# Optimization experiments

Hardware: AMD Instinct MI355X
Metric: run time of the kernel (lower is better)

The kernel has to match this reference:

```python
import math
import jax, jax.numpy as jnp
import numpy as np

# ---------- static Cl(3,0,0) algebra tables ----------
_BLADES = [(), (1,), (2,), (3,), (1, 2), (1, 3), (2, 3), (1, 2, 3)]
N_BLADES = 8
SUBSPACES = np.array([1, 3, 3, 1])
GRADE = np.array([len(b) for b in _BLADES])  # blade index -> grade

def _blade_mul(a, b):
    idx = list(a) + list(b)
    sign = 1
    changed = True
    while changed:
        changed = False
        for t in range(len(idx) - 1):
            if idx[t] > idx[t + 1]:
                idx[t], idx[t + 1] = idx[t + 1], idx[t]
                sign = -sign
                changed = True
    out = []
    t = 0
    while t < len(idx):
        if t + 1 < len(idx) and idx[t] == idx[t + 1]:
            t += 2  # e_i e_i = +1 (Euclidean metric)
        else:
            out.append(idx[t]); t += 1
    return sign, tuple(out)

# cayley[i, j, k]: e_i * e_k contributes sign to blade j (matches einsum 'bni,nijk,bnk->bnj')
CAYLEY = np.zeros((N_BLADES, N_BLADES, N_BLADES), dtype=np.float32)
for i, ba in enumerate(_BLADES):
    for k, bb in enumerate(_BLADES):
        s, res = _blade_mul(ba, bb)
        CAYLEY[i, _BLADES.index(res), k] = s

_starts = np.concatenate([[0], np.cumsum(SUBSPACES)[:-1]])
_paths = np.zeros((4, 4, 4), dtype=bool)
for gi in range(4):
    for gj in range(4):
        for gk in range(4):
            si, sj, sk = _starts[gi], _starts[gj], _starts[gk]
            blk = CAYLEY[si:si + SUBSPACES[gi], sj:sj + SUBSPACES[gj], sk:sk + SUBSPACES[gk]]
            _paths[gi, gj, gk] = np.any(blk != 0)
_grade_idx = np.argwhere(_paths)  # row-major order, matches torch.nonzero
N_PATHS = len(_grade_idx)  # 20 for Cl(3,0)

_bi, _bj, _bk, _pidx, _cv = [], [], [], [], []
for p, (gi, gj, gk) in enumerate(_grade_idx):
    for bi in range(_starts[gi], _starts[gi] + SUBSPACES[gi]):
        for bj in range(_starts[gj], _starts[gj] + SUBSPACES[gj]):
            for bk in range(_starts[gk], _starts[gk] + SUBSPACES[gk]):
                c = CAYLEY[bi, bj, bk]
                if c != 0:
                    _bi.append(bi); _bj.append(bj); _bk.append(bk)
                    _pidx.append(p); _cv.append(c)
BI = np.array(_bi); BJ = np.array(_bj); BK = np.array(_bk)
PIDX = np.array(_pidx); CV = np.array(_cv, dtype=np.float32)  # E = 64 nonzero entries

G_ONEHOT = (GRADE[:, None] == np.arange(4)[None, :]).astype(np.float32)  # (8, 4)

B, N_IN, N_OUT = 2048, 512, 512
EPS = 1e-6

def setup_inputs() -> dict:
    key = jax.random.key(0)
    k = jax.random.split(key, 6)
    x = jax.random.normal(k[0], (B, N_IN, N_BLADES), jnp.float32)
    weight = jax.random.normal(k[1], (N_OUT, N_IN, N_PATHS), jnp.float32) / math.sqrt(N_IN * 4)
    w_right = jax.random.normal(k[2], (N_IN, N_IN, 4), jnp.float32) / math.sqrt(N_IN)
    w_left = jax.random.normal(k[3], (N_OUT, N_IN, 4), jnp.float32) / math.sqrt(N_IN)
    b_left = jax.random.normal(k[4], (N_OUT,), jnp.float32) * 0.01
    norm_a = jnp.zeros((1, N_IN, 4), jnp.float32)  # normalization_init = 0
    return dict(x=x, weight=weight, w_right=w_right, w_left=w_left, b_left=b_left, norm_a=norm_a)

def _mvlinear(x, w):
    # w: (out, in, n_grades) -> per-blade weight via grade lookup (repeat_interleave)
    return jnp.einsum('bni,mni->bmi', x, w[:, :, GRADE])

def reference(x, weight, w_right, w_left, b_left, norm_a):
    # linear_right (no bias)
    xr = _mvlinear(x, w_right)
    # NormalizationLayer: per-grade norm, sigmoid-gated rescale toward 1
    norms = jnp.sqrt(jnp.einsum('bni,ig->bng', xr * xr, G_ONEHOT))  # (B, n, 4)
    factor = jax.nn.sigmoid(norm_a) * (norms - 1.0) + 1.0
    xr = xr / (factor[:, :, GRADE] + EPS)
    # sparse bilinear geometric product: only the 64 nonzero cayley entries
    pair = x[:, :, BI] * xr[:, :, BK]            # (B, n, E)
    wsel = weight[:, :, PIDX] * CV               # (m, n, E)
    tmp = jnp.einsum('bne,mne->bme', pair, wsel)  # (B, m, E)
    bilinear = jnp.zeros((x.shape[0], weight.shape[0], N_BLADES), x.dtype).at[:, :, BJ].add(tmp)
    # linear_left with bias embedded on the scalar blade (index 0)
    left = _mvlinear(x, w_left).at[:, :, 0].add(b_left)
    return (left + bilinear) / math.sqrt(2.0)
```

## Files before the change

### kernel.cpp

```cpp
#include <hip/hip_runtime.h>
#include <stdint.h>


#define B_DIM 2048
#define N_DIM 512
#define PLANE (B_DIM * N_DIM)
#define WPLANE (N_DIM * N_DIM)
#define KTOT (9 * N_DIM)
#define TILE_US (128 * 32)

using frag8 = __attribute__((ext_vector_type(8))) short;
using f32x4 = __attribute__((ext_vector_type(4))) float;

__device__ __forceinline__ float bf2f(unsigned short u) {
  union { unsigned int i; float f; } v;
  v.i = ((unsigned int)u) << 16;
  return v.f;
}
__device__ __forceinline__ unsigned short f2bf(float f) {
  unsigned int u = __float_as_uint(f);
  return (unsigned short)((u + 0x7FFFu + ((u >> 16) & 1u)) >> 16);
}
__device__ __forceinline__ unsigned int pairpack(unsigned int a, unsigned int r) {
  const float pe = __uint_as_float(a << 16) * __uint_as_float(r << 16);
  const float po = __uint_as_float(a & 0xFFFF0000u) * __uint_as_float(r & 0xFFFF0000u);
  return __builtin_amdgcn_perm(__float_as_uint(po) + 0x8000u,
                               __float_as_uint(pe) + 0x8000u, 0x07060302u);
}

typedef const unsigned int __attribute__((address_space(1)))* gas_t;
typedef unsigned int __attribute__((address_space(3)))* las_t;
__device__ __forceinline__ void gload16(const void* g, void* l) {
  __builtin_amdgcn_global_load_lds((gas_t)g, (las_t)l, 16, 0, 0);
}

#define PIPE_FENCE(N)                                                  \
  do {                                                                 \
    asm volatile("s_waitcnt vmcnt(" #N ") lgkmcnt(0)" ::: "memory");   \
    __builtin_amdgcn_s_barrier();                                      \
    __builtin_amdgcn_sched_barrier(0);                                 \
  } while (0)

#define SGN_INIT {                                                     \
  {0,0,0,0,0x8000,0x8000,0x8000,0x8000},                               \
  {0,0,0,0,0x8000,0x8000,0x8000,0x8000},                               \
  {0,0x8000,0,0,0,0,0x8000,0},                                         \
  {0,0x8000,0x8000,0,0x8000,0,0,0x8000},                               \
  {0,0x8000,0,0,0,0,0x8000,0},                                         \
  {0,0x8000,0x8000,0,0x8000,0,0,0x8000},                               \
  {0,0,0x8000,0,0,0x8000,0,0},                                         \
  {0,0,0x8000,0,0,0x8000,0,0} }
#define PJK_INIT {                                                     \
  {0,4,4,4,10,10,10,16},  {5,1,11,11,6,6,17,12},                       \
  {5,11,1,11,6,17,6,12},  {5,11,11,1,17,6,6,12},                       \
  {13,7,7,18,2,14,14,8},  {13,7,18,7,14,2,14,8},                       \
  {13,18,7,7,14,14,2,8},  {19,15,15,15,9,9,9,3} }
#define GR_INIT {0,1,1,1,2,2,2,3}


__global__ __launch_bounds__(256) void repack_x(const float* __restrict__ x,
                                                unsigned short* __restrict__ xt) {
  const int t = blockIdx.x * 256 + threadIdx.x;
  const float4 v0 = *(const float4*)(x + (size_t)t * 8);
  const float4 v1 = *(const float4*)(x + (size_t)t * 8 + 4);
  const float v[8] = {v0.x, v0.y, v0.z, v0.w, v1.x, v1.y, v1.z, v1.w};
#pragma unroll
  for (int i = 0; i < 8; ++i) xt[(size_t)i * PLANE + t] = f2bf(v[i]);
}

__global__ __launch_bounds__(256) void repack_wr(const float* __restrict__ wr,
                                                 unsigned short* __restrict__ wrt) {
  const int t = blockIdx.x * 256 + threadIdx.x;
  const float4 v = *(const float4*)(wr + (size_t)t * 4);
  const float p[4] = {v.x, v.y, v.z, v.w};
#pragma unroll
  for (int g = 0; g < 4; ++g) wrt[(size_t)g * WPLANE + t] = f2bf(p[g]);
}

__global__ __launch_bounds__(256) void build_W(const float* __restrict__ w,
                                               const float* __restrict__ wl,
                                               unsigned short* __restrict__ Wall) {
  constexpr int PJK[8][8] = PJK_INIT;
  constexpr unsigned short SGN[8][8] = SGN_INIT;
  constexpr int GR[8] = GR_INIT;
  const int t = blockIdx.x * 256 + threadIdx.x;
  const int m = t >> 9, n = t & 511;
  const float* wrow = w + (size_t)t * 20;
  const float* wlrow = wl + (size_t)t * 4;
  unsigned short w20[20];
#pragma unroll
  for (int p = 0; p < 20; ++p) w20[p] = f2bf(wrow[p]);
  unsigned short wl4[4];
#pragma unroll
  for (int g = 0; g < 4; ++g) wl4[g] = f2bf(wlrow[g]);
#pragma unroll
  for (int j = 0; j < 8; ++j) {
    const size_t base = ((size_t)j * N_DIM + m) * KTOT + n;
#pragma unroll
    for (int k = 0; k < 8; ++k)
      Wall[base + (size_t)k * N_DIM] = (unsigned short)(w20[PJK[j][k]] ^ SGN[j][k]);
    Wall[base + (size_t)8 * N_DIM] = wl4[GR[j]];
  }
}

__global__ __launch_bounds__(256) void normk(unsigned short* __restrict__ xre,
                                             const float* __restrict__ na) {
  const int t = blockIdx.x * 256 + threadIdx.x;
  const int n = t & 511;
  float v[8];
#pragma unroll
  for (int p = 0; p < 8; ++p) v[p] = bf2f(xre[(size_t)p * PLANE + t]);
  const float n0 = fabsf(v[0]);
  const float n1 = sqrtf(v[1] * v[1] + v[2] * v[2] + v[3] * v[3]);
  const float n2 = sqrtf(v[4] * v[4] + v[5] * v[5] + v[6] * v[6]);
  const float n3 = fabsf(v[7]);
  float f[4];
  const float nm[4] = {n0, n1, n2, n3};
#pragma unroll
  for (int g = 0; g < 4; ++g) {
    const float a = na[n * 4 + g];
    const float sig = 1.0f / (1.0f + __expf(-a));
    f[g] = sig * (nm[g] - 1.0f) + 1.0f + 1e-6f;
  }
  v[0] /= f[0];
  v[1] /= f[1]; v[2] /= f[1]; v[3] /= f[1];
  v[4] /= f[2]; v[5] /= f[2]; v[6] /= f[2];
  v[7] /= f[3];
#pragma unroll
  for (int p = 0; p < 8; ++p) xre[(size_t)p * PLANE + t] = f2bf(v[p]);
  xre[(size_t)8 * PLANE + t] = 0x3F80;
}


__global__ __launch_bounds__(512, 4) void gemm1(const unsigned short* __restrict__ xt,
                                                const unsigned short* __restrict__ wrt,
                                                unsigned short* __restrict__ xre) {
  constexpr int GR[8] = GR_INIT;
  __shared__ unsigned short sA[2][TILE_US];
  __shared__ unsigned short sB[2][TILE_US];
  const int bm0 = blockIdx.x * 128, bn0 = blockIdx.y * 128, z = blockIdx.z;
  const unsigned short* A = xt + (size_t)z * PLANE;
  const unsigned short* Bm = wrt + (size_t)GR[z] * WPLANE;
  unsigned short* C = xre + (size_t)z * PLANE;

  const int tid = (int)threadIdx.x;
  const int lane = tid & 63, wave = tid >> 6;
  const int wm = (wave >> 2) * 64, wn = (wave & 3) * 32;
  const int fr = lane & 15, quad = lane >> 4;
  const int row = tid >> 2;
  const int ks = (((tid & 3) ^ ((tid >> 3) & 3))) * 8;
  const int wbase = wave * 512;

  const unsigned short* pa = A + (size_t)(bm0 + row) * N_DIM + ks;
  const unsigned short* pb = Bm + (size_t)(bn0 + row) * N_DIM + ks;

  const int msw = (fr >> 1) & 3;
  const int rdA = (wm + fr) * 32 + (quad ^ msw) * 8;
  const int rdB = (wn + fr) * 32 + (quad ^ msw) * 8;

  f32x4 acc[4][2];
#pragma unroll
  for (int mt = 0; mt < 4; ++mt)
#pragma unroll
    for (int nt = 0; nt < 2; ++nt) acc[mt][nt] = (f32x4){0.f, 0.f, 0.f, 0.f};

  gload16(pa, &sA[0][wbase]);
  gload16(pb, &sB[0][wbase]);
  PIPE_FENCE(0);

  for (int it = 0; it < 16; ++it) {
    const int c = it & 1;
    if (it < 15) {
      gload16(pa + ((it + 1) << 5), &sA[c ^ 1][wbase]);
      gload16(pb + ((it + 1) << 5), &sB[c ^ 1][wbase]);
    }
    frag8 af[4], bfr[2];
#pragma unroll
    for (int t = 0; t < 4; ++t) af[t] = *(const frag8*)&sA[c][rdA + t * 512];
#pragma unroll
    for (int t = 0; t < 2; ++t) bfr[t] = *(const frag8*)&sB[c][rdB + t * 512];
#pragma unroll
    for (int mt = 0; mt < 4; ++mt)
#pragma unroll
      for (int nt = 0; nt < 2; ++nt)
        acc[mt][nt] = __builtin_amdgcn_mfma_f32_16x16x32_bf16(af[mt], bfr[nt], acc[mt][nt], 0, 0, 0);
    if (it < 15) PIPE_FENCE(0);
  }
#pragma unroll
  for (int mt = 0; mt < 4; ++mt) {
    const int row0 = bm0 + wm + mt * 16 + quad * 4;
#pragma unroll
    for (int nt = 0; nt < 2; ++nt) {
      const int col = bn0 + wn + nt * 16 + fr;
#pragma unroll
      for (int r = 0; r < 4; ++r)
        C[(size_t)(row0 + r) * N_DIM + col] = f2bf(acc[mt][nt][r]);
    }
  }
}


__global__ __launch_bounds__(512, 4) void gemm2(const unsigned short* __restrict__ xt,
                                                const unsigned short* __restrict__ xre,
                                                const unsigned short* __restrict__ Wall,
                                                const float* __restrict__ bl,
                                                float* __restrict__ out) {
  __shared__ unsigned short sA[2][TILE_US];
  __shared__ unsigned short sB3[3][TILE_US];
  const int bm0 = blockIdx.x * 128, bn0 = blockIdx.y * 128, j = blockIdx.z;

  const int tid = (int)threadIdx.x;
  const int lane = tid & 63, wave = tid >> 6;
  const int wm = (wave >> 2) * 64, wn = (wave & 3) * 32;
  const int fr = lane & 15, quad = lane >> 4;
  const int row = tid >> 2, k8 = (tid & 3) * 8;
  const int ks = (((tid & 3) ^ ((tid >> 3) & 3))) * 8;
  const int wbase = wave * 512;
  const int pj = (j == 3 || j == 4) ? (j ^ 7) : j;

  f32x4 acc[4][2];
#pragma unroll
  for (int mt = 0; mt < 4; ++mt)
#pragma unroll
    for (int nt = 0; nt < 2; ++nt) acc[mt][nt] = (f32x4){0.f, 0.f, 0.f, 0.f};

  const size_t arow = (size_t)(bm0 + row) * N_DIM + k8;
  const unsigned short* pwb = Wall + ((size_t)j * N_DIM + bn0 + row) * KTOT + ks;

  auto ieof = [&](int sl) -> int {
    int ps = (sl == 3 || sl == 4) ? (sl ^ 7) : sl;
    int ix = pj ^ ps;
    ix = (ix == 3 || ix == 4) ? (ix ^ 7) : ix;
    return (sl == 8) ? j : ix;
  };

  const int msw = (fr >> 1) & 3;
  const int rdA = (wm + fr) * 32 + (quad ^ msw) * 8;
  const int rdB = (wn + fr) * 32 + (quad ^ msw) * 8;
  const int wrA = row * 32 + ks;

  {
    uint4 rx = *(const uint4*)(xt + ((size_t)ieof(0) << 20) + arow);
    uint4 rr = *(const uint4*)(xre + arow);
    gload16(pwb, &sB3[0][wbase]);
    gload16(pwb + 32, &sB3[1][wbase]);
    uint4 o;
    o.x = pairpack(rx.x, rr.x);
    o.y = pairpack(rx.y, rr.y);
    o.z = pairpack(rx.z, rr.z);
    o.w = pairpack(rx.w, rr.w);
    *(uint4*)&sA[0][wrA] = o;
  }
  PIPE_FENCE(1);

  uint4 rx, rr;
  int cb = 0, wb = 2;
  for (int it = 0; it < 144; ++it) {
    const int c2 = it & 1;
    if (it < 143) {
      const int kn = it + 1;
      const int slk = kn >> 4, n0k = (kn & 15) << 5;
      int ps = (slk == 3 || slk == 4) ? (slk ^ 7) : slk;
      int ix = pj ^ ps;
      ix = (ix == 3 || ix == 4) ? (ix ^ 7) : ix;
      const int ie = (slk == 8) ? j : ix;
      rx = *(const uint4*)(xt + ((size_t)ie << 20) + arow + n0k);
      rr = *(const uint4*)(xre + ((size_t)slk << 20) + arow + n0k);
      if (it < 142) gload16(pwb + (size_t)(it + 2) * 32, &sB3[wb][wbase]);
    }
    frag8 af[4], bfr[2];
#pragma unroll
    for (int t = 0; t < 4; ++t) af[t] = *(const frag8*)&sA[c2][rdA + t * 512];
#pragma unroll
    for (int t = 0; t < 2; ++t) bfr[t] = *(const frag8*)&sB3[cb][rdB + t * 512];
#pragma unroll
    for (int mt = 0; mt < 4; ++mt)
#pragma unroll
      for (int nt = 0; nt < 2; ++nt)
        acc[mt][nt] = __builtin_amdgcn_mfma_f32_16x16x32_bf16(af[mt], bfr[nt], acc[mt][nt], 0, 0, 0);
    if (it < 143) {
      uint4 o;
      o.x = pairpack(rx.x, rr.x);
      o.y = pairpack(rx.y, rr.y);
      o.z = pairpack(rx.z, rr.z);
      o.w = pairpack(rx.w, rr.w);
      *(uint4*)&sA[c2 ^ 1][wrA] = o;
      PIPE_FENCE(1);
    }
    cb = (cb + 1 == 3) ? 0 : cb + 1;
    wb = (wb + 1 == 3) ? 0 : wb + 1;
  }

  const float inv = 0.70710678118654752f;
#pragma unroll
  for (int nt = 0; nt < 2; ++nt) {
    const int col = bn0 + wn + nt * 16 + fr;
    const float bias = (j == 0) ? bl[col] : 0.0f;
#pragma unroll
    for (int mt = 0; mt < 4; ++mt) {
      const int row0 = bm0 + wm + mt * 16 + quad * 4;
#pragma unroll
      for (int r = 0; r < 4; ++r)
        out[((size_t)(row0 + r) * N_DIM + col) * 8 + j] =
            (acc[mt][nt][r] + bias) * inv;
    }
  }
}


extern "C" void kernel_launch(void* const* d_in, const int* in_sizes, int n_in,
                              void* d_out, int out_size, void* d_ws, size_t ws_size,
                              hipStream_t stream) {
  const float* x = (const float*)d_in[0];
  const float* w = (const float*)d_in[1];
  const float* wr = (const float*)d_in[2];
  const float* wl = (const float*)d_in[3];
  const float* bl = (const float*)d_in[4];
  const float* na = (const float*)d_in[5];
  float* out = (float*)d_out;

  char* ws = (char*)d_ws;
  unsigned short* xt = (unsigned short*)(ws);
  unsigned short* xre = (unsigned short*)(ws + 16777216);
  unsigned short* wrt = (unsigned short*)(ws + 35651584);
  unsigned short* Wall = (unsigned short*)(ws + 37748736);

  repack_x<<<4096, 256, 0, stream>>>(x, xt);
  repack_wr<<<1024, 256, 0, stream>>>(wr, wrt);
  build_W<<<1024, 256, 0, stream>>>(w, wl, Wall);
  gemm1<<<dim3(16, 4, 8), 512, 0, stream>>>(xt, wrt, xre);
  normk<<<4096, 256, 0, stream>>>(xre, na);
  gemm2<<<dim3(16, 4, 8), 512, 0, stream>>>(xt, xre, Wall, bl, out);
}
```

Measured before the change: 309.7 us.

## Deepen prefetch pipelines in both GEMMs to hide global load latency

Both GEMM kernels move from double/triple buffering to a four-slot LDS ring for the streamed operand, prefetching three K-steps ahead with relaxed vmcnt waits. gemm2 also loads the activation pair operands two steps ahead through registers. The fence macro drops the compiler sched_barrier so instructions can be scheduled across the barrier. This aims to hide global memory latency behind MFMA work, at the cost of more LDS per block (which may reduce occupancy), more live registers, and fragile hand-counted wait values.

```diff
diff --git a/kernel.cpp b/kernel.cpp
--- a/kernel.cpp
+++ b/kernel.cpp
@@ -34,12 +34,8 @@
   __builtin_amdgcn_global_load_lds((gas_t)g, (las_t)l, 16, 0, 0);
 }
 
-#define PIPE_FENCE(N)                                                  \
-  do {                                                                 \
-    asm volatile("s_waitcnt vmcnt(" #N ") lgkmcnt(0)" ::: "memory");   \
-    __builtin_amdgcn_s_barrier();                                      \
-    __builtin_amdgcn_sched_barrier(0);                                 \
-  } while (0)
+#define PIPE_FENCE(N)                                                       \
+  asm volatile("s_waitcnt vmcnt(" #N ") lgkmcnt(0)\n\ts_barrier" ::: "memory")
 
 #define SGN_INIT {                                                     \
   {0,0,0,0,0x8000,0x8000,0x8000,0x8000},                               \
@@ -136,8 +132,8 @@
                                                 const unsigned short* __restrict__ wrt,
                                                 unsigned short* __restrict__ xre) {
   constexpr int GR[8] = GR_INIT;
-  __shared__ unsigned short sA[2][TILE_US];
-  __shared__ unsigned short sB[2][TILE_US];
+  __shared__ __attribute__((aligned(16))) unsigned short sA4[4][TILE_US];
+  __shared__ __attribute__((aligned(16))) unsigned short sB4[4][TILE_US];
   const int bm0 = blockIdx.x * 128, bn0 = blockIdx.y * 128, z = blockIdx.z;
   const unsigned short* A = xt + (size_t)z * PLANE;
   const unsigned short* Bm = wrt + (size_t)GR[z] * WPLANE;
@@ -164,27 +160,30 @@
 #pragma unroll
     for (int nt = 0; nt < 2; ++nt) acc[mt][nt] = (f32x4){0.f, 0.f, 0.f, 0.f};
 
-  gload16(pa, &sA[0][wbase]);
-  gload16(pb, &sB[0][wbase]);
-  PIPE_FENCE(0);
-
+  gload16(pa, &sA4[0][wbase]);       gload16(pb, &sB4[0][wbase]);
+  gload16(pa + 32, &sA4[1][wbase]);  gload16(pb + 32, &sB4[1][wbase]);
+  gload16(pa + 64, &sA4[2][wbase]);  gload16(pb + 64, &sB4[2][wbase]);
+  PIPE_FENCE(4);
+
+#pragma unroll 2
   for (int it = 0; it < 16; ++it) {
-    const int c = it & 1;
-    if (it < 15) {
-      gload16(pa + ((it + 1) << 5), &sA[c ^ 1][wbase]);
-      gload16(pb + ((it + 1) << 5), &sB[c ^ 1][wbase]);
+    if (it < 13) {
+      gload16(pa + ((it + 3) << 5), &sA4[(it + 3) & 3][wbase]);
+      gload16(pb + ((it + 3) << 5), &sB4[(it + 3) & 3][wbase]);
     }
     frag8 af[4], bfr[2];
 #pragma unroll
-    for (int t = 0; t < 4; ++t) af[t] = *(const frag8*)&sA[c][rdA + t * 512];
-#pragma unroll
-    for (int t = 0; t < 2; ++t) bfr[t] = *(const frag8*)&sB[c][rdB + t * 512];
+    for (int t = 0; t < 4; ++t) af[t] = *(const frag8*)&sA4[it & 3][rdA + t * 512];
+#pragma unroll
+    for (int t = 0; t < 2; ++t) bfr[t] = *(const frag8*)&sB4[it & 3][rdB + t * 512];
 #pragma unroll
     for (int mt = 0; mt < 4; ++mt)
 #pragma unroll
       for (int nt = 0; nt < 2; ++nt)
         acc[mt][nt] = __builtin_amdgcn_mfma_f32_16x16x32_bf16(af[mt], bfr[nt], acc[mt][nt], 0, 0, 0);
-    if (it < 15) PIPE_FENCE(0);
+    if (it < 13) PIPE_FENCE(4);
+    else if (it == 13) PIPE_FENCE(2);
+    else if (it == 14) PIPE_FENCE(0);
   }
 #pragma unroll
   for (int mt = 0; mt < 4; ++mt) {
@@ -205,8 +204,8 @@
                                                 const unsigned short* __restrict__ Wall,
                                                 const float* __restrict__ bl,
                                                 float* __restrict__ out) {
-  __shared__ unsigned short sA[2][TILE_US];
-  __shared__ unsigned short sB3[3][TILE_US];
+  __shared__ __attribute__((aligned(16))) unsigned short sA2[2][TILE_US];
+  __shared__ __attribute__((aligned(16))) unsigned short sB4[4][TILE_US];
   const int bm0 = blockIdx.x * 128, bn0 = blockIdx.y * 128, j = blockIdx.z;
 
   const int tid = (int)threadIdx.x;
@@ -239,56 +238,64 @@
   const int rdB = (wn + fr) * 32 + (quad ^ msw) * 8;
   const int wrA = row * 32 + ks;
 
+  uint4 rxP, rrP;
   {
-    uint4 rx = *(const uint4*)(xt + ((size_t)ieof(0) << 20) + arow);
-    uint4 rr = *(const uint4*)(xre + arow);
-    gload16(pwb, &sB3[0][wbase]);
-    gload16(pwb + 32, &sB3[1][wbase]);
+    const uint4 r0x = *(const uint4*)(xt + ((size_t)ieof(0) << 20) + arow);
+    const uint4 r0r = *(const uint4*)(xre + arow);
+    gload16(pwb, &sB4[0][wbase]);
+    gload16(pwb + 32, &sB4[1][wbase]);
+    gload16(pwb + 64, &sB4[2][wbase]);
+    rxP = *(const uint4*)(xt + ((size_t)ieof(0) << 20) + arow + 32);
+    rrP = *(const uint4*)(xre + arow + 32);
     uint4 o;
-    o.x = pairpack(rx.x, rr.x);
-    o.y = pairpack(rx.y, rr.y);
-    o.z = pairpack(rx.z, rr.z);
-    o.w = pairpack(rx.w, rr.w);
-    *(uint4*)&sA[0][wrA] = o;
-  }
-  PIPE_FENCE(1);
-
-  uint4 rx, rr;
-  int cb = 0, wb = 2;
+    o.x = pairpack(r0x.x, r0r.x);
+    o.y = pairpack(r0x.y, r0r.y);
+    o.z = pairpack(r0x.z, r0r.z);
+    o.w = pairpack(r0x.w, r0r.w);
+    *(uint4*)&sA2[0][wrA] = o;
+  }
+  PIPE_FENCE(4);
+
+#pragma unroll 2
   for (int it = 0; it < 144; ++it) {
     const int c2 = it & 1;
-    if (it < 143) {
-      const int kn = it + 1;
+    uint4 rxN, rrN;
+    if (it < 142) {
+      const int kn = it + 2;
       const int slk = kn >> 4, n0k = (kn & 15) << 5;
       int ps = (slk == 3 || slk == 4) ? (slk ^ 7) : slk;
       int ix = pj ^ ps;
       ix = (ix == 3 || ix == 4) ? (ix ^ 7) : ix;
       const int ie = (slk == 8) ? j : ix;
-      rx = *(const uint4*)(xt + ((size_t)ie << 20) + arow + n0k);
-      rr = *(const uint4*)(xre + ((size_t)slk << 20) + arow + n0k);
-      if (it < 142) gload16(pwb + (size_t)(it + 2) * 32, &sB3[wb][wbase]);
-    }
+      rxN = *(const uint4*)(xt + ((size_t)ie << 20) + arow + n0k);
+      rrN = *(const uint4*)(xre + ((size_t)slk << 20) + arow + n0k);
+    }
+    if (it < 141) gload16(pwb + (size_t)(it + 3) * 32, &sB4[(it + 3) & 3][wbase]);
+
     frag8 af[4], bfr[2];
 #pragma unroll
-    for (int t = 0; t < 4; ++t) af[t] = *(const frag8*)&sA[c2][rdA + t * 512];
-#pragma unroll
-    for (int t = 0; t < 2; ++t) bfr[t] = *(const frag8*)&sB3[cb][rdB + t * 512];
+    for (int t = 0; t < 4; ++t) af[t] = *(const frag8*)&sA2[c2][rdA + t * 512];
+#pragma unroll
+    for (int t = 0; t < 2; ++t) bfr[t] = *(const frag8*)&sB4[it & 3][rdB + t * 512];
 #pragma unroll
     for (int mt = 0; mt < 4; ++mt)
 #pragma unroll
       for (int nt = 0; nt < 2; ++nt)
         acc[mt][nt] = __builtin_amdgcn_mfma_f32_16x16x32_bf16(af[mt], bfr[nt], acc[mt][nt], 0, 0, 0);
+
     if (it < 143) {
       uint4 o;
-      o.x = pairpack(rx.x, rr.x);
-      o.y = pairpack(rx.y, rr.y);
-      o.z = pairpack(rx.z, rr.z);
-      o.w = pairpack(rx.w, rr.w);
-      *(uint4*)&sA[c2 ^ 1][wrA] = o;
-      PIPE_FENCE(1);
-    }
-    cb = (cb + 1 == 3) ? 0 : cb + 1;
-    wb = (wb + 1 == 3) ? 0 : wb + 1;
+      o.x = pairpack(rxP.x, rrP.x);
+      o.y = pairpack(rxP.y, rrP.y);
+      o.z = pairpack(rxP.z, rrP.z);
+      o.w = pairpack(rxP.w, rrP.w);
+      *(uint4*)&sA2[c2 ^ 1][wrA] = o;
+    }
+    rxP = rxN;
+    rrP = rrN;
+    if (it < 141) PIPE_FENCE(4);
+    else if (it == 141) PIPE_FENCE(3);
+    else if (it == 142) PIPE_FENCE(0);
   }
 
   const float inv = 0.70710678118654752f;
```

Result: no change. 305.6 us (-1.3%).
